# Optimization experiments

Hardware: AMD Instinct MI355X
Metric: run time of the kernel (lower is better)

The kernel has to match this reference:

```python
import jax, jax.numpy as jnp
import numpy as np

B, N, L = 256, 4096, 6
EMBED, HID, VOCAB = 16, 32, 200
NOTE, LSTM_D, T = 64, 64, 128


def _tree_structure():
    """One random tree of N nodes (root=node 0), tiled across the batch.
    height = distance above deepest descendant; children have strictly smaller height."""
    rng = np.random.default_rng(0)
    height = np.zeros(N, np.int32)
    height[0] = L
    height[1:] = rng.integers(0, L, N - 1)
    kind = np.full(N, 2, np.int32)  # 2 = internal
    leaf_mask = height == 0
    kind[leaf_mask] = (rng.random(leaf_mask.sum()) < 0.1).astype(np.int32)  # 1=ptr, 0=leaf
    parent = np.zeros(N, np.int64)
    for hl in range(L):
        mask = height == hl
        cand = np.where((height > hl) & (kind == 2))[0]  # root always qualifies
        parent[mask] = rng.choice(cand, size=int(mask.sum()))
    parent[0] = 0  # root points to itself; harmless (its own h stays 0 until final level)
    return height, kind, parent


def setup_inputs():
    height, kind, parent = _tree_structure()
    offs = (np.arange(B, dtype=np.int64) * N)[:, None]
    rng = np.random.default_rng(1)
    inp = {
        'kind': jnp.asarray(np.tile(kind, B), jnp.int32),
        'height': jnp.asarray(np.tile(height, B), jnp.int32),
        'parent': jnp.asarray((parent[None, :] + offs).reshape(-1), jnp.int32),
        'tok_a': jnp.asarray(rng.integers(0, VOCAB, B * N), jnp.int32),
        'tok_b': jnp.asarray(rng.integers(0, VOCAB, B * N), jnp.int32),
        'ptr_time': jnp.asarray(rng.integers(0, T, B * N), jnp.int32),
    }
    key = jax.random.key(0)
    ks = jax.random.split(key, 16)
    def w(k, shape, scale=0.05):
        return (jax.random.normal(k, shape, jnp.float32) * scale)
    inp['first_notes'] = w(ks[0], (B, NOTE), 1.0)
    inp['lstm_out'] = w(ks[1], (B, T, LSTM_D), 1.0)
    inp['embedding'] = w(ks[2], (VOCAB, EMBED), 0.02)
    inp['leaf_w1'] = w(ks[3], (2 * EMBED, HID)); inp['leaf_b1'] = w(ks[4], (HID,))
    inp['leaf_w2'] = w(ks[5], (HID, HID));       inp['leaf_b2'] = w(ks[6], (HID,))
    inp['node_w'] = w(ks[7], (2 * EMBED + HID, HID)); inp['node_b'] = w(ks[8], (HID,))
    inp['ptr_w'] = w(ks[9], (NOTE + LSTM_D, HID));    inp['ptr_b'] = w(ks[10], (HID,))
    inp['ff_w1'] = w(ks[11], (HID, HID)); inp['ff_b1'] = w(ks[12], (HID,))
    inp['ff_w2'] = w(ks[13], (HID, HID)); inp['ff_b2'] = w(ks[14], (HID,))
    inp['tail_w'] = w(ks[15], (HID, 1)); inp['tail_b'] = jnp.zeros((1,), jnp.float32)
    return inp


def reference(kind, height, parent, tok_a, tok_b, ptr_time, first_notes, lstm_out,
              embedding, leaf_w1, leaf_b1, leaf_w2, leaf_b2, node_w, node_b,
              ptr_w, ptr_b, ff_w1, ff_b1, ff_w2, ff_b2, tail_w, tail_b):
    M = kind.shape[0]
    nb = first_notes.shape[0]
    n_per = M // nb
    tree_id = jnp.arange(M, dtype=jnp.int32) // n_per
    emb_a = embedding[tok_a]  # [M, EMBED] (parent-type / first-token embed)
    emb_b = embedding[tok_b]  # [M, EMBED] (node-type / second-token embed)
    pair = jnp.concatenate([emb_a, emb_b], axis=-1)  # [M, 2*EMBED]
    # leaf path: two stacked linears (no nonlinearity), as in leaf_ff
    leaf_h = (pair @ leaf_w1 + leaf_b1) @ leaf_w2 + leaf_b2
    # ptr path: Linear(note_dim + lstm_out_dim -> hidden)
    ptr_in = jnp.concatenate([first_notes[tree_id], lstm_out[tree_id, ptr_time]], axis=-1)
    ptr_h = ptr_in @ ptr_w + ptr_b
    h = jnp.where((kind == 0)[:, None], leaf_h,
                  jnp.where((kind == 1)[:, None], ptr_h, 0.0))
    # level-synchronous child-sum: children always have smaller height
    for lvl in range(1, L + 1):
        csum = jax.ops.segment_sum(h, parent, num_segments=M)  # [M, HID]
        inner = jax.nn.relu(jnp.concatenate([pair, csum], axis=-1) @ node_w + node_b)
        h = jnp.where((height == lvl)[:, None], inner, h)
    roots = h[::n_per]  # [B, HID], root is node 0 of each tree block
    ff = (roots @ ff_w1 + ff_b1) @ ff_w2 + ff_b2
    return ff @ tail_w + tail_b  # [B, 1]


if __name__ == '__main__':
    out = reference(**setup_inputs())
    print(out.shape, out.dtype)
```

## Files before the change

### kernel.cpp

```cpp
#include <hip/hip_runtime.h>

#define BATCH   256
#define N_PER   4096
#define EMBED   16
#define HID     32
#define NOTE    64
#define LSTM_D  64
#define T_LEN   128
#define VOCAB   200
#define HSTR    (BATCH * HID)

#define MH_C0    0
#define MH_C1    1
#define MH_CNT   2
#define MH_P     7
#define MH_PBASE 8
#define OFF_K0N   64
#define OFF_K0S   (OFF_K0N + N_PER)
#define OFF_K1N   (OFF_K0S + N_PER)
#define OFF_K1S   (OFF_K1N + N_PER)
#define OFF_PLIST (OFF_K1S + N_PER)
#define OFF_WSLOT (OFF_PLIST + N_PER)
#define OFF_COFF  (OFF_WSLOT + N_PER)
#define EAW_OFF     (1024 * 1024)
#define EBW_OFF     (EAW_OFF + VOCAB * HID * 4)
#define LA2_OFF     (EBW_OFF + VOCAB * HID * 4)
#define LB2_OFF     (LA2_OFF + VOCAB * HID * 4)
#define CC_OFF      (LB2_OFF + VOCAB * HID * 4)
#define H_OFF       (8ull * 1024 * 1024)

__device__ __forceinline__ unsigned long long shflup64(unsigned long long x, int off) {
    unsigned lo = (unsigned)(x & 0xffffffffull);
    unsigned hi = (unsigned)(x >> 32);
    lo = __shfl_up(lo, off, 64);
    hi = __shfl_up(hi, off, 64);
    return ((unsigned long long)hi << 32) | (unsigned long long)lo;
}

__global__ __launch_bounds__(1024) void build_structure(
    const int* __restrict__ kind, const int* __restrict__ height,
    const int* __restrict__ parent, int* __restrict__ meta,
    const float* __restrict__ embedding,
    const float* __restrict__ leaf_w1, const float* __restrict__ leaf_b1,
    const float* __restrict__ leaf_w2, const float* __restrict__ leaf_b2,
    const float* __restrict__ node_w,
    float* __restrict__ eaw_g, float* __restrict__ ebw_g,
    float* __restrict__ la2, float* __restrict__ lb2, float* __restrict__ cc)
{
    __shared__ unsigned long long wlo[16], whi[16];
    __shared__ int wint[16];
    __shared__ int node2pidx[N_PER];
    __shared__ int deg[N_PER];
    __shared__ int sbases[8];
    __shared__ int stot[8];

    int t  = threadIdx.x;
    int i0 = 4 * t;
    int laneid = t & 63;
    int wid    = t >> 6;

    int par[4], hgt4[4], kn4[4];
    #pragma unroll
    for (int q = 0; q < 4; ++q) {
        par[q]  = parent[i0 + q];
        hgt4[q] = height[i0 + q];
        kn4[q]  = kind[i0 + q];
    }

    int myb[4];
    #pragma unroll
    for (int q = 0; q < 4; ++q) {
        int hgt = hgt4[q];
        int b;
        if (hgt > 0) { b = 1 + hgt; if (b > 7) b = 7; }
        else b = (kn4[q] == 0) ? 0 : 1;
        myb[q] = b;
    }
    unsigned long long clo = 0, chi = 0;
    #pragma unroll
    for (int q = 0; q < 4; ++q) {
        int b = myb[q];
        if (b < 4) clo += 1ull << (16 * b);
        else       chi += 1ull << (16 * (b - 4));
    }

    unsigned long long a = clo, b64 = chi;
    #pragma unroll
    for (int off = 1; off < 64; off <<= 1) {
        unsigned long long ua = shflup64(a, off);
        unsigned long long ub = shflup64(b64, off);
        if (laneid >= off) { a += ua; b64 += ub; }
    }
    if (laneid == 63) { wlo[wid] = a; whi[wid] = b64; }
    __syncthreads();
    unsigned long long blo = 0, bhi = 0;
    for (int w = 0; w < wid; ++w) { blo += wlo[w]; bhi += whi[w]; }
    unsigned long long inc_lo = a + blo, inc_hi = b64 + bhi;
    if (t == 0) {
        unsigned long long tlo = 0, thi = 0;
        for (int w = 0; w < 16; ++w) { tlo += wlo[w]; thi += whi[w]; }
        stot[0] = (int)(tlo & 0xFFFF);         stot[1] = (int)((tlo >> 16) & 0xFFFF);
        stot[2] = (int)((tlo >> 32) & 0xFFFF); stot[3] = (int)((tlo >> 48) & 0xFFFF);
        stot[4] = (int)(thi & 0xFFFF);         stot[5] = (int)((thi >> 16) & 0xFFFF);
        stot[6] = (int)((thi >> 32) & 0xFFFF); stot[7] = (int)((thi >> 48) & 0xFFFF);
        int s = 0;
        for (int bb = 0; bb < 8; ++bb) { sbases[bb] = s; s += stot[bb]; }
        meta[MH_C0] = stot[0];
        meta[MH_C1] = stot[1];
        for (int l = 0; l < 5; ++l) meta[MH_CNT + l]   = stot[2 + l];
        for (int l = 0; l < 5; ++l) meta[MH_PBASE + l] = sbases[2 + l] - sbases[2];
        meta[MH_P] = (sbases[7] - sbases[2]) + stot[7];
    }
    __syncthreads();

    unsigned long long exlo = inc_lo - clo, exhi = inc_hi - chi;
    int mypos[4], mypidx[4];
    #pragma unroll
    for (int q = 0; q < 4; ++q) {
        int i = i0 + q, b = myb[q];
        int pos;
        if (b < 4) { pos = (int)((exlo >> (16 * b)) & 0xFFFF); exlo += 1ull << (16 * b); }
        else       { pos = (int)((exhi >> (16 * (b - 4))) & 0xFFFF); exhi += 1ull << (16 * (b - 4)); }
        mypos[q] = pos;
        int pidx = -1;
        if (b == 0)      meta[OFF_K0N + pos] = i;
        else if (b == 1) meta[OFF_K1N + pos] = i;
        else {
            pidx = (sbases[b] - sbases[2]) + pos;
            meta[OFF_PLIST + pidx] = i;
            node2pidx[i] = pidx;
        }
        mypidx[q] = pidx;
    }
    #pragma unroll
    for (int q = 0; q < 4; ++q) deg[i0 + q] = 0;
    __syncthreads();

    #pragma unroll
    for (int q = 0; q < 4; ++q) {
        int i = i0 + q;
        if (i != 0) atomicAdd(&deg[node2pidx[par[q]]], 1);
    }
    __syncthreads();

    int d0 = deg[i0], d1 = deg[i0 + 1], d2 = deg[i0 + 2], d3 = deg[i0 + 3];
    int s4 = d0 + d1 + d2 + d3;

    int vi = s4;
    #pragma unroll
    for (int off = 1; off < 64; off <<= 1) {
        int u = __shfl_up(vi, off, 64);
        if (laneid >= off) vi += u;
    }
    if (laneid == 63) wint[wid] = vi;
    __syncthreads();
    int bint = 0;
    for (int w = 0; w < wid; ++w) bint += wint[w];
    int incl = vi + bint;

    int ex = incl - s4;
    int o0 = ex, o1 = ex + d0, o2 = o1 + d1, o3 = o2 + d2;
    deg[i0] = o0; deg[i0 + 1] = o1; deg[i0 + 2] = o2; deg[i0 + 3] = o3;
    meta[OFF_COFF + i0]     = o0;
    meta[OFF_COFF + i0 + 1] = o1;
    meta[OFF_COFF + i0 + 2] = o2;
    meta[OFF_COFF + i0 + 3] = o3;
    if (t == 1023) meta[OFF_COFF + N_PER] = o3 + d3;
    __syncthreads();

    #pragma unroll
    for (int q = 0; q < 4; ++q) {
        int i = i0 + q; if (i == 0) continue;
        int slot = atomicAdd(&deg[node2pidx[par[q]]], 1);
        int b = myb[q];
        if (b == 0)      meta[OFF_K0S + mypos[q]] = slot;
        else if (b == 1) meta[OFF_K1S + mypos[q]] = slot;
        else             meta[OFF_WSLOT + mypidx[q]] = slot;
    }

    {
        int hw = t >> 5, ln = t & 31;
        for (int v = hw; v < VOCAB; v += 32) {
            const float* ev = embedding + v * EMBED;
            float ea = 0.f, eb = 0.f, t1a = 0.f, t1b = 0.f;
            #pragma unroll
            for (int k = 0; k < EMBED; ++k) {
                float e = ev[k];
                ea  += e * node_w[k * HID + ln];
                eb  += e * node_w[(EMBED + k) * HID + ln];
                t1a += e * leaf_w1[k * HID + ln];
                t1b += e * leaf_w1[(EMBED + k) * HID + ln];
            }
            eaw_g[v * HID + ln] = ea;
            ebw_g[v * HID + ln] = eb;
            float a2 = 0.f, b2v = 0.f;
            #pragma unroll
            for (int k = 0; k < HID; ++k) {
                float w2 = leaf_w2[k * HID + ln];
                a2  += __shfl(t1a, k, 32) * w2;
                b2v += __shfl(t1b, k, 32) * w2;
            }
            la2[v * HID + ln] = a2;
            lb2[v * HID + ln] = b2v;
        }
        if (t < HID) {
            float c = leaf_b2[t];
            #pragma unroll
            for (int k = 0; k < HID; ++k) c += leaf_b1[k] * leaf_w2[k * HID + t];
            cc[t] = c;
        }
    }
}

__global__ __launch_bounds__(1024) void tree_kernel(
    const int* __restrict__ meta,
    const int* __restrict__ tok_a, const int* __restrict__ tok_b,
    const int* __restrict__ ptr_time,
    const float* __restrict__ first_notes, const float* __restrict__ lstm_out,
    const float* __restrict__ la2, const float* __restrict__ lb2,
    const float* __restrict__ cc,
    const float* __restrict__ ptr_w, const float* __restrict__ ptr_b,
    const float* __restrict__ eaw_g, const float* __restrict__ ebw_g,
    const float* __restrict__ node_w, const float* __restrict__ node_b,
    const float* __restrict__ ff_w1, const float* __restrict__ ff_b1,
    const float* __restrict__ ff_w2, const float* __restrict__ ff_b2,
    const float* __restrict__ tail_w, const float* __restrict__ tail_b,
    float* __restrict__ h, float* __restrict__ out)
{
    __shared__ float pw[(NOTE + LSTM_D) * HID];
    __shared__ float wlds[HID * HID];
    __shared__ float fnl[NOTE];
    __shared__ float part[16][33];

    int t    = threadIdx.x;
    int lane = t & 31;
    int g    = t >> 5;
    int tree = blockIdx.x;

    for (int x = t; x < (NOTE + LSTM_D) * HID; x += 1024) pw[x] = ptr_w[x];
    for (int x = t; x < HID * HID; x += 1024) wlds[x] = node_w[2 * EMBED * HID + x];
    if (t < NOTE) fnl[t] = first_notes[(size_t)tree * NOTE + t];
    __syncthreads();

    const int* K0N = meta + OFF_K0N;
    const int* K0S = meta + OFF_K0S;
    const int* K1N = meta + OFF_K1N;
    const int* K1S = meta + OFF_K1S;
    const int* PL  = meta + OFF_PLIST;
    const int* WS  = meta + OFF_WSLOT;
    const int* CO  = meta + OFF_COFF;

    {
        float ccv = cc[lane];
        int c0 = meta[MH_C0];
        for (int j = g; j < c0; j += 32) {
            int nd = K0N[j], slot = K0S[j];
            int gn = tree * N_PER + nd;
            int ta = tok_a[gn], tb = tok_b[gn];
            h[(size_t)slot * HSTR + tree * HID + lane] =
                ccv + la2[ta * HID + lane] + lb2[tb * HID + lane];
        }
    }

    {
        float pb = ptr_b[lane];
        int c1 = meta[MH_C1];
        for (int j = g; j < c1; j += 32) {
            int nd = K1N[j], slot = K1S[j];
            int gn = tree * N_PER + nd;
            int tt = ptr_time[gn];
            const float* lo = lstm_out + ((size_t)tree * T_LEN + tt) * LSTM_D;
            float v = pb;
            #pragma unroll
            for (int k = 0; k < NOTE; ++k)   v += fnl[k] * pw[k * HID + lane];
            #pragma unroll
            for (int k = 0; k < LSTM_D; ++k) v += lo[k] * pw[(NOTE + k) * HID + lane];
            h[(size_t)slot * HSTR + tree * HID + lane] = v;
        }
    }
    __syncthreads();

    float nb = node_b[lane];
    for (int lvl = 0; lvl < 5; ++lvl) {
        int cnt   = meta[MH_CNT + lvl];
        int pbase = meta[MH_PBASE + lvl];
        for (int pp = g; pp < cnt; pp += 32) {
            int pidx = pbase + pp;
            int node = PL[pidx], wslot = WS[pidx];
            int e0 = CO[pidx], e1 = CO[pidx + 1];

            int gn = tree * N_PER + node;
            int ta = tok_a[gn], tb = tok_b[gn];

            float csum = 0.f;
            const float* hb = h + (size_t)tree * HID + lane;
            for (int c = e0; c < e1; ++c) csum += hb[(size_t)c * HSTR];

            float v = nb + eaw_g[ta * HID + lane] + ebw_g[tb * HID + lane];
            #pragma unroll
            for (int k = 0; k < HID; ++k)
                v += __shfl(csum, k, 32) * wlds[k * HID + lane];
            h[(size_t)wslot * HSTR + tree * HID + lane] = fmaxf(v, 0.f);
        }
        __syncthreads();
    }

    {
        int P = meta[MH_P];
        int e = CO[P - 1], e1 = CO[P];
        const float* hb = h + (size_t)tree * HID + lane;
        if (g < 16) {
            float s = 0.f;
            for (int c = e + g; c < e1; c += 16)
                s += hb[(size_t)c * HSTR];
            part[g][lane] = s;
        }
        __syncthreads();

        if (g == 0) {
            float csum = part[0][lane];
            #pragma unroll
            for (int k = 1; k < 16; ++k) csum += part[k][lane];

            int gn = tree * N_PER;
            int ta = tok_a[gn], tb = tok_b[gn];
            float v = nb + eaw_g[ta * HID + lane] + ebw_g[tb * HID + lane];
            #pragma unroll
            for (int k = 0; k < HID; ++k)
                v += __shfl(csum, k, 32) * wlds[k * HID + lane];
            v = fmaxf(v, 0.f);

            float f1 = ff_b1[lane];
            #pragma unroll
            for (int k = 0; k < HID; ++k) f1 += __shfl(v, k, 32) * ff_w1[k * HID + lane];
            float f2 = ff_b2[lane];
            #pragma unroll
            for (int k = 0; k < HID; ++k) f2 += __shfl(f1, k, 32) * ff_w2[k * HID + lane];

            float c2 = f2 * tail_w[lane];
            #pragma unroll
            for (int off = 16; off > 0; off >>= 1) c2 += __shfl_down(c2, off, 32);
            if (lane == 0) out[tree] = c2 + tail_b[0];
        }
    }
}

extern "C" void kernel_launch(void* const* d_in, const int* in_sizes, int n_in,
                              void* d_out, int out_size, void* d_ws, size_t ws_size,
                              hipStream_t stream) {
    const int*   kind        = (const int*)d_in[0];
    const int*   height      = (const int*)d_in[1];
    const int*   parent      = (const int*)d_in[2];
    const int*   tok_a       = (const int*)d_in[3];
    const int*   tok_b       = (const int*)d_in[4];
    const int*   ptr_time    = (const int*)d_in[5];
    const float* first_notes = (const float*)d_in[6];
    const float* lstm_out    = (const float*)d_in[7];
    const float* embedding   = (const float*)d_in[8];
    const float* leaf_w1     = (const float*)d_in[9];
    const float* leaf_b1     = (const float*)d_in[10];
    const float* leaf_w2     = (const float*)d_in[11];
    const float* leaf_b2     = (const float*)d_in[12];
    const float* node_w      = (const float*)d_in[13];
    const float* node_b      = (const float*)d_in[14];
    const float* ptr_w       = (const float*)d_in[15];
    const float* ptr_b       = (const float*)d_in[16];
    const float* ff_w1       = (const float*)d_in[17];
    const float* ff_b1       = (const float*)d_in[18];
    const float* ff_w2       = (const float*)d_in[19];
    const float* ff_b2       = (const float*)d_in[20];
    const float* tail_w      = (const float*)d_in[21];
    const float* tail_b      = (const float*)d_in[22];

    char* ws = (char*)d_ws;
    int*   meta    = (int*)ws;
    float* eaw_g   = (float*)(ws + EAW_OFF);
    float* ebw_g   = (float*)(ws + EBW_OFF);
    float* la2     = (float*)(ws + LA2_OFF);
    float* lb2     = (float*)(ws + LB2_OFF);
    float* cc      = (float*)(ws + CC_OFF);
    float* h       = (float*)(ws + H_OFF);

    build_structure<<<1, 1024, 0, stream>>>(
        kind, height, parent, meta,
        embedding, leaf_w1, leaf_b1, leaf_w2, leaf_b2, node_w,
        eaw_g, ebw_g, la2, lb2, cc);

    tree_kernel<<<BATCH, 1024, 0, stream>>>(
        meta, tok_a, tok_b, ptr_time, first_notes, lstm_out,
        la2, lb2, cc, ptr_w, ptr_b, eaw_g, ebw_g, node_w, node_b,
        ff_w1, ff_b1, ff_w2, ff_b2, tail_w, tail_b,
        h, (float*)d_out);
}
```

Baseline: 404.4 us.

## Switch h buffer to per-tree contiguous layout and batch four nodes per warp

Changes the intermediate h storage from slot-major interleaved across trees to tree-major, so each block's child rows are contiguous within its own region. This improves cache locality for the child-sum gathers. The leaf and internal-node loops now process four nodes per 32-lane group, issuing their index and token loads together and sharing each weight LDS read across four accumulators to raise memory-level parallelism. The cost is more registers per thread and extra idle iterations when the four nodes have uneven child counts.

```diff
diff --git a/kernel.cpp b/kernel.cpp
--- a/kernel.cpp
+++ b/kernel.cpp
@@ -8,7 +8,7 @@
 #define LSTM_D  64
 #define T_LEN   128
 #define VOCAB   200
-#define HSTR    (BATCH * HID)
+#define TSTR    (N_PER * HID)
 
 #define MH_C0    0
 #define MH_C1    1
@@ -250,15 +250,27 @@
     const int* WS  = meta + OFF_WSLOT;
     const int* CO  = meta + OFF_COFF;
 
+    float* ht = h + (size_t)tree * TSTR;
+
     {
         float ccv = cc[lane];
         int c0 = meta[MH_C0];
-        for (int j = g; j < c0; j += 32) {
-            int nd = K0N[j], slot = K0S[j];
-            int gn = tree * N_PER + nd;
-            int ta = tok_a[gn], tb = tok_b[gn];
-            h[(size_t)slot * HSTR + tree * HID + lane] =
-                ccv + la2[ta * HID + lane] + lb2[tb * HID + lane];
+        for (int base = g * 4; base < c0; base += 128) {
+            int nq = c0 - base; if (nq > 4) nq = 4;
+            int sl[4], ta[4], tb[4];
+            #pragma unroll
+            for (int q = 0; q < 4; ++q) {
+                int j = base + (q < nq ? q : 0);
+                int nd = K0N[j]; sl[q] = K0S[j];
+                int gn = tree * N_PER + nd;
+                ta[q] = tok_a[gn]; tb[q] = tok_b[gn];
+            }
+            #pragma unroll
+            for (int q = 0; q < 4; ++q) {
+                if (q >= nq) break;
+                ht[sl[q] * HID + lane] =
+                    ccv + la2[ta[q] * HID + lane] + lb2[tb[q] * HID + lane];
+            }
         }
     }
 
@@ -275,7 +287,7 @@
             for (int k = 0; k < NOTE; ++k)   v += fnl[k] * pw[k * HID + lane];
             #pragma unroll
             for (int k = 0; k < LSTM_D; ++k) v += lo[k] * pw[(NOTE + k) * HID + lane];
-            h[(size_t)slot * HSTR + tree * HID + lane] = v;
+            ht[slot * HID + lane] = v;
         }
     }
     __syncthreads();
@@ -284,23 +296,49 @@
     for (int lvl = 0; lvl < 5; ++lvl) {
         int cnt   = meta[MH_CNT + lvl];
         int pbase = meta[MH_PBASE + lvl];
-        for (int pp = g; pp < cnt; pp += 32) {
-            int pidx = pbase + pp;
-            int node = PL[pidx], wslot = WS[pidx];
-            int e0 = CO[pidx], e1 = CO[pidx + 1];
-
-            int gn = tree * N_PER + node;
-            int ta = tok_a[gn], tb = tok_b[gn];
-
-            float csum = 0.f;
-            const float* hb = h + (size_t)tree * HID + lane;
-            for (int c = e0; c < e1; ++c) csum += hb[(size_t)c * HSTR];
-
-            float v = nb + eaw_g[ta * HID + lane] + ebw_g[tb * HID + lane];
-            #pragma unroll
-            for (int k = 0; k < HID; ++k)
-                v += __shfl(csum, k, 32) * wlds[k * HID + lane];
-            h[(size_t)wslot * HSTR + tree * HID + lane] = fmaxf(v, 0.f);
+        for (int base = g * 4; base < cnt; base += 128) {
+            int nq = cnt - base; if (nq > 4) nq = 4;
+            int ws[4], e0[4], nch[4], ta[4], tb[4];
+            #pragma unroll
+            for (int q = 0; q < 4; ++q) {
+                int pidx = pbase + base + (q < nq ? q : 0);
+                int nd = PL[pidx];
+                ws[q] = WS[pidx];
+                e0[q] = CO[pidx];
+                nch[q] = CO[pidx + 1] - e0[q];
+                if (q >= nq) nch[q] = 0;
+                int gn = tree * N_PER + nd;
+                ta[q] = tok_a[gn]; tb[q] = tok_b[gn];
+            }
+            int mx = nch[0];
+            #pragma unroll
+            for (int q = 1; q < 4; ++q) mx = nch[q] > mx ? nch[q] : mx;
+
+            float cs[4] = {0.f, 0.f, 0.f, 0.f};
+            for (int c = 0; c < mx; ++c) {
+                #pragma unroll
+                for (int q = 0; q < 4; ++q)
+                    if (c < nch[q]) cs[q] += ht[(e0[q] + c) * HID + lane];
+            }
+
+            float v[4];
+            #pragma unroll
+            for (int q = 0; q < 4; ++q)
+                v[q] = nb + eaw_g[ta[q] * HID + lane] + ebw_g[tb[q] * HID + lane];
+
+            #pragma unroll
+            for (int k = 0; k < HID; ++k) {
+                float w = wlds[k * HID + lane];
+                #pragma unroll
+                for (int q = 0; q < 4; ++q)
+                    v[q] += __shfl(cs[q], k, 32) * w;
+            }
+
+            #pragma unroll
+            for (int q = 0; q < 4; ++q) {
+                if (q >= nq) break;
+                ht[ws[q] * HID + lane] = fmaxf(v[q], 0.f);
+            }
         }
         __syncthreads();
     }
@@ -308,11 +346,10 @@
     {
         int P = meta[MH_P];
         int e = CO[P - 1], e1 = CO[P];
-        const float* hb = h + (size_t)tree * HID + lane;
         if (g < 16) {
             float s = 0.f;
             for (int c = e + g; c < e1; c += 16)
-                s += hb[(size_t)c * HSTR];
+                s += ht[c * HID + lane];
             part[g][lane] = s;
         }
         __syncthreads();
```

After: 1.246 ms. 208% more time.
